# Kernel optimization log

Measured on AMD Instinct MI355X. Metric: run time of the kernel, lower is better.

Reference implementation:

```python
import jax, jax.numpy as jnp
import numpy as np

IN_NODES, OUT_NODES, F_SIZE = 4096, 1024, 16


def setup_inputs() -> dict:
    key = jax.random.key(0)
    u_hat = jax.random.normal(key, (IN_NODES * OUT_NODES, F_SIZE), dtype=jnp.float32)
    return {"u_hat": u_hat, "routing_num": 3}


def squash(s):
    # s: [out, f]
    sq = jnp.sum(s * s, axis=1, keepdims=True)
    return sq / (1.0 + sq) * (s / jnp.sqrt(sq))


def reference(u_hat, routing_num):
    # u_hat laid out edge-major as (in_node, out_node) blocks, matching DGL edge order
    uh = u_hat.reshape(IN_NODES, OUT_NODES, F_SIZE)
    b0 = jnp.zeros((IN_NODES, OUT_NODES), dtype=u_hat.dtype)

    def step(b, _):
        c = jax.nn.softmax(b, axis=1)                 # coupling coeffs over out capsules
        s = jnp.einsum('io,iof->of', c, uh)           # weighted message sum per out node
        v = squash(s)                                 # [out, f]
        b = b + jnp.einsum('iof,of->io', uh, v)       # agreement b-update
        return b, v

    _, vs = jax.lax.scan(step, b0, None, length=routing_num)
    return vs[-1]  # final out-capsule activations [OUT_NODES, F_SIZE]
```

## Files before the change

### kernel.cpp

```cpp
#include <hip/hip_runtime.h>
#include <math.h>

#define IN_NODES  4096
#define OUT_NODES 1024
#define FSZ       16
#define ROW_ELEMS (OUT_NODES * FSZ)

__device__ __forceinline__ float dot4(const float4 a, const float4 b) {
    return a.x*b.x + a.y*b.y + a.z*b.z + a.w*b.w;
}
__device__ __forceinline__ void fma4(float4& a, const float c, const float4 u) {
    a.x += c*u.x; a.y += c*u.y; a.z += c*u.z; a.w += c*u.w;
}
__device__ __forceinline__ void add4(float4& a, const float4 u) {
    a.x += u.x; a.y += u.y; a.z += u.z; a.w += u.w;
}

template <bool UNIFORM>
__global__ __launch_bounds__(1024) void route_pass(const float* __restrict__ uh,
                                                   const float* __restrict__ V,
                                                   float* __restrict__ s_partial,
                                                   int per_block) {
    const int t    = threadIdx.x;
    const int wave = t >> 6;
    const int lane = t & 63;
    const int c4   = (wave << 8) + lane;

    __shared__ float2 redw[16];
    __shared__ float2 redS;

    float4 v0, v1, v2, v3;
    if (!UNIFORM) {
        const float4* vp = reinterpret_cast<const float4*>(V) + c4;
        v0 = vp[0]; v1 = vp[64]; v2 = vp[128]; v3 = vp[192];
    }

    float4 a0 = make_float4(0.f,0.f,0.f,0.f), a1 = a0, a2 = a0, a3 = a0;

    const int i0 = blockIdx.x * per_block;
    for (int g = 0; g < per_block; g += 2) {
        const float4* pa = reinterpret_cast<const float4*>(
                               uh + (size_t)(i0 + g) * ROW_ELEMS) + c4;
        const float4* pb = pa + (ROW_ELEMS / 4);
        float4 ua0 = pa[0], ua1 = pa[64], ua2 = pa[128], ua3 = pa[192];
        float4 ub0 = pb[0], ub1 = pb[64], ub2 = pb[128], ub3 = pb[192];

        if (UNIFORM) {
            add4(a0, ua0); add4(a0, ub0);
            add4(a1, ua1); add4(a1, ub1);
            add4(a2, ua2); add4(a2, ub2);
            add4(a3, ua3); add4(a3, ub3);
        } else {
            float da0 = dot4(ua0, v0), da1 = dot4(ua1, v1),
                  da2 = dot4(ua2, v2), da3 = dot4(ua3, v3);
            float db0 = dot4(ub0, v0), db1 = dot4(ub1, v1),
                  db2 = dot4(ub2, v2), db3 = dot4(ub3, v3);
            da0 += __shfl_xor(da0, 1); da0 += __shfl_xor(da0, 2);
            da1 += __shfl_xor(da1, 1); da1 += __shfl_xor(da1, 2);
            da2 += __shfl_xor(da2, 1); da2 += __shfl_xor(da2, 2);
            da3 += __shfl_xor(da3, 1); da3 += __shfl_xor(da3, 2);
            db0 += __shfl_xor(db0, 1); db0 += __shfl_xor(db0, 2);
            db1 += __shfl_xor(db1, 1); db1 += __shfl_xor(db1, 2);
            db2 += __shfl_xor(db2, 1); db2 += __shfl_xor(db2, 2);
            db3 += __shfl_xor(db3, 1); db3 += __shfl_xor(db3, 2);

            float ea0 = __expf(da0), ea1 = __expf(da1),
                  ea2 = __expf(da2), ea3 = __expf(da3);
            float eb0 = __expf(db0), eb1 = __expf(db1),
                  eb2 = __expf(db2), eb3 = __expf(db3);

            float sx = (ea0 + ea1) + (ea2 + ea3);
            float sy = (eb0 + eb1) + (eb2 + eb3);
            #pragma unroll
            for (int off = 32; off; off >>= 1) {
                sx += __shfl_xor(sx, off);
                sy += __shfl_xor(sy, off);
            }
            if (lane == 0) redw[wave] = make_float2(sx, sy);
            __syncthreads();
            if (wave == 0) {
                float2 q = (lane < 16) ? redw[lane] : make_float2(0.f, 0.f);
                #pragma unroll
                for (int off = 8; off; off >>= 1) {
                    q.x += __shfl_xor(q.x, off);
                    q.y += __shfl_xor(q.y, off);
                }
                if (lane == 0) redS = q;
            }
            __syncthreads();
            const float inva = 4.0f / redS.x;
            const float invb = 4.0f / redS.y;

            fma4(a0, ea0 * inva, ua0); fma4(a0, eb0 * invb, ub0);
            fma4(a1, ea1 * inva, ua1); fma4(a1, eb1 * invb, ub1);
            fma4(a2, ea2 * inva, ua2); fma4(a2, eb2 * invb, ub2);
            fma4(a3, ea3 * inva, ua3); fma4(a3, eb3 * invb, ub3);
        }
    }

    if (UNIFORM) {
        const float c = 1.0f / OUT_NODES;
        a0.x*=c; a0.y*=c; a0.z*=c; a0.w*=c;
        a1.x*=c; a1.y*=c; a1.z*=c; a1.w*=c;
        a2.x*=c; a2.y*=c; a2.z*=c; a2.w*=c;
        a3.x*=c; a3.y*=c; a3.z*=c; a3.w*=c;
    }

    float4* sp = reinterpret_cast<float4*>(
                     s_partial + (size_t)blockIdx.x * ROW_ELEMS) + c4;
    sp[0] = a0; sp[64] = a1; sp[128] = a2; sp[192] = a3;
}

__global__ __launch_bounds__(256) void reduce_squash(const float* __restrict__ s_partial,
                                                     float* __restrict__ V,
                                                     float* __restrict__ out,
                                                     int nblk, int first) {
    const int gidx = blockIdx.x * 256 + threadIdx.x;
    float s0 = 0.f, s1 = 0.f, s2 = 0.f, s3 = 0.f;
    int b = 0;
    for (; b + 3 < nblk; b += 4) {
        s0 += s_partial[(size_t)(b    ) * ROW_ELEMS + gidx];
        s1 += s_partial[(size_t)(b + 1) * ROW_ELEMS + gidx];
        s2 += s_partial[(size_t)(b + 2) * ROW_ELEMS + gidx];
        s3 += s_partial[(size_t)(b + 3) * ROW_ELEMS + gidx];
    }
    for (; b < nblk; ++b)
        s0 += s_partial[(size_t)b * ROW_ELEMS + gidx];
    float s = (s0 + s1) + (s2 + s3);

    float sq = s * s;
    #pragma unroll
    for (int m = 8; m; m >>= 1)
        sq += __shfl_xor(sq, m);

    float scale = sq / ((1.0f + sq) * sqrtf(sq));
    float v = s * scale;

    out[gidx] = v;
    V[gidx]   = first ? v : (V[gidx] + v);
}

extern "C" void kernel_launch(void* const* d_in, const int* in_sizes, int n_in,
                              void* d_out, int out_size, void* d_ws, size_t ws_size,
                              hipStream_t stream) {
    const float* uh  = (const float*)d_in[0];
    float*       out = (float*)d_out;

    char*  ws   = (char*)d_ws;
    float* V    = (float*)ws;
    float* part = (float*)(ws + 65536);

    int G = 256;
    while (G > 1 && ws_size < 65536ull * (size_t)(G + 1)) G >>= 1;
    const int per_block = IN_NODES / G;

    route_pass<true><<<G, 1024, 0, stream>>>(uh, V, part, per_block);
    reduce_squash<<<64, 256, 0, stream>>>(part, V, out, G, 1);

    for (int t = 1; t < 3; ++t) {
        route_pass<false><<<G, 1024, 0, stream>>>(uh, V, part, per_block);
        reduce_squash<<<64, 256, 0, stream>>>(part, V, out, G, 0);
    }
}
```

Measured before the change: 195.9 us.

## Stream a bf16 copy of u_hat for the softmax routing passes

The first (uniform) pass now also writes a bf16 copy of u_hat into the workspace. The two later softmax-weighted passes read that half-size copy instead of the fp32 input, with register double-buffering of the next rows. The goal is to cut HBM traffic on the passes limited by memory bandwidth. The cost is an extra 128MB write in pass one and bf16 rounding error in the dot products and weighted sums. If the workspace is too small, the code falls back to the fp32 path.

Result: no change. 197.3 us (+0.7%).

```diff
diff --git a/kernel.cpp b/kernel.cpp
--- a/kernel.cpp
+++ b/kernel.cpp
@@ -3,8 +3,11 @@
 
 #define IN_NODES  4096
 #define OUT_NODES 1024
-#define FSZ       16
-#define ROW_ELEMS (OUT_NODES * FSZ)
+#define ROW_ELEMS (OUT_NODES * 16)
+#define ROW_C4    (ROW_ELEMS / 4)
+
+typedef unsigned short u16;
+typedef unsigned int   u32;
 
 __device__ __forceinline__ float dot4(const float4 a, const float4 b) {
     return a.x*b.x + a.y*b.y + a.z*b.z + a.w*b.w;
@@ -15,12 +18,60 @@
 __device__ __forceinline__ void add4(float4& a, const float4 u) {
     a.x += u.x; a.y += u.y; a.z += u.z; a.w += u.w;
 }
-
-template <bool UNIFORM>
-__global__ __launch_bounds__(1024) void route_pass(const float* __restrict__ uh,
-                                                   const float* __restrict__ V,
-                                                   float* __restrict__ s_partial,
-                                                   int per_block) {
+__device__ __forceinline__ float b2f1(u16 u) {
+    return __uint_as_float(((u32)u) << 16);
+}
+__device__ __forceinline__ float4 b2f(ushort4 u) {
+    return make_float4(b2f1(u.x), b2f1(u.y), b2f1(u.z), b2f1(u.w));
+}
+__device__ __forceinline__ u16 f2b(float x) {
+    u32 b = __float_as_uint(x);
+    return (u16)((b + 0x7FFFu + ((b >> 16) & 1u)) >> 16);
+}
+__device__ __forceinline__ ushort4 f2b4(float4 v) {
+    ushort4 r; r.x = f2b(v.x); r.y = f2b(v.y); r.z = f2b(v.z); r.w = f2b(v.w);
+    return r;
+}
+
+template <bool WBF16>
+__global__ __launch_bounds__(1024) void route_uniform(const float* __restrict__ uh,
+                                                      float* __restrict__ s_partial,
+                                                      u16* __restrict__ uh2,
+                                                      int per_block) {
+    const int t  = threadIdx.x;
+    const int c4 = ((t >> 6) << 8) + (t & 63);
+
+    float4 a0 = make_float4(0.f,0.f,0.f,0.f), a1 = a0, a2 = a0, a3 = a0;
+
+    const int i0 = blockIdx.x * per_block;
+    const float4* p = reinterpret_cast<const float4*>(uh) + (size_t)i0 * ROW_C4 + c4;
+    ushort4*      q = reinterpret_cast<ushort4*>(uh2)     + (size_t)i0 * ROW_C4 + c4;
+
+    for (int g = 0; g < per_block; ++g) {
+        float4 u0 = p[0], u1 = p[64], u2 = p[128], u3 = p[192];
+        add4(a0, u0); add4(a1, u1); add4(a2, u2); add4(a3, u3);
+        if (WBF16) {
+            q[0]   = f2b4(u0); q[64]  = f2b4(u1);
+            q[128] = f2b4(u2); q[192] = f2b4(u3);
+            q += ROW_C4;
+        }
+        p += ROW_C4;
+    }
+
+    const float c = 1.0f / OUT_NODES;
+    a0.x*=c; a0.y*=c; a0.z*=c; a0.w*=c;
+    a1.x*=c; a1.y*=c; a1.z*=c; a1.w*=c;
+    a2.x*=c; a2.y*=c; a2.z*=c; a2.w*=c;
+    a3.x*=c; a3.y*=c; a3.z*=c; a3.w*=c;
+
+    float4* sp = reinterpret_cast<float4*>(s_partial) + (size_t)blockIdx.x * ROW_C4 + c4;
+    sp[0] = a0; sp[64] = a1; sp[128] = a2; sp[192] = a3;
+}
+
+__global__ __launch_bounds__(1024) void route_soft_bf16(const u16* __restrict__ uh2,
+                                                        const float* __restrict__ V,
+                                                        float* __restrict__ s_partial,
+                                                        int per_block) {
     const int t    = threadIdx.x;
     const int wave = t >> 6;
     const int lane = t & 63;
@@ -29,85 +80,158 @@
     __shared__ float2 redw[16];
     __shared__ float2 redS;
 
-    float4 v0, v1, v2, v3;
-    if (!UNIFORM) {
-        const float4* vp = reinterpret_cast<const float4*>(V) + c4;
-        v0 = vp[0]; v1 = vp[64]; v2 = vp[128]; v3 = vp[192];
-    }
+    const float4* vp = reinterpret_cast<const float4*>(V) + c4;
+    const float4 v0 = vp[0], v1 = vp[64], v2 = vp[128], v3 = vp[192];
+
+    float4 a0 = make_float4(0.f,0.f,0.f,0.f), a1 = a0, a2 = a0, a3 = a0;
+
+    const ushort4* p = reinterpret_cast<const ushort4*>(uh2)
+                     + (size_t)(blockIdx.x * per_block) * ROW_C4 + c4;
+
+    ushort4 ca0 = p[0], ca1 = p[64], ca2 = p[128], ca3 = p[192];
+    const ushort4* pb = p + ROW_C4;
+    ushort4 cb0 = pb[0], cb1 = pb[64], cb2 = pb[128], cb3 = pb[192];
+
+    for (int g = 0; g < per_block; g += 2) {
+        ushort4 na0, na1, na2, na3, nb0, nb1, nb2, nb3;
+        const ushort4* pn = p + 2 * ROW_C4;
+        if (g + 2 < per_block) {
+            na0 = pn[0]; na1 = pn[64]; na2 = pn[128]; na3 = pn[192];
+            const ushort4* pn2 = pn + ROW_C4;
+            nb0 = pn2[0]; nb1 = pn2[64]; nb2 = pn2[128]; nb3 = pn2[192];
+        }
+
+        const float4 fa0 = b2f(ca0), fa1 = b2f(ca1), fa2 = b2f(ca2), fa3 = b2f(ca3);
+        const float4 fb0 = b2f(cb0), fb1 = b2f(cb1), fb2 = b2f(cb2), fb3 = b2f(cb3);
+
+        float da0 = dot4(fa0, v0), da1 = dot4(fa1, v1),
+              da2 = dot4(fa2, v2), da3 = dot4(fa3, v3);
+        float db0 = dot4(fb0, v0), db1 = dot4(fb1, v1),
+              db2 = dot4(fb2, v2), db3 = dot4(fb3, v3);
+
+        da0 += __shfl_xor(da0, 1); da0 += __shfl_xor(da0, 2);
+        da1 += __shfl_xor(da1, 1); da1 += __shfl_xor(da1, 2);
+        da2 += __shfl_xor(da2, 1); da2 += __shfl_xor(da2, 2);
+        da3 += __shfl_xor(da3, 1); da3 += __shfl_xor(da3, 2);
+        db0 += __shfl_xor(db0, 1); db0 += __shfl_xor(db0, 2);
+        db1 += __shfl_xor(db1, 1); db1 += __shfl_xor(db1, 2);
+        db2 += __shfl_xor(db2, 1); db2 += __shfl_xor(db2, 2);
+        db3 += __shfl_xor(db3, 1); db3 += __shfl_xor(db3, 2);
+
+        float ea0 = __expf(da0), ea1 = __expf(da1),
+              ea2 = __expf(da2), ea3 = __expf(da3);
+        float eb0 = __expf(db0), eb1 = __expf(db1),
+              eb2 = __expf(db2), eb3 = __expf(db3);
+
+        float sx = (ea0 + ea1) + (ea2 + ea3);
+        float sy = (eb0 + eb1) + (eb2 + eb3);
+        #pragma unroll
+        for (int off = 32; off; off >>= 1) {
+            sx += __shfl_xor(sx, off);
+            sy += __shfl_xor(sy, off);
+        }
+        if (lane == 0) redw[wave] = make_float2(sx, sy);
+        __syncthreads();
+        if (wave == 0) {
+            float2 qv = (lane < 16) ? redw[lane] : make_float2(0.f, 0.f);
+            #pragma unroll
+            for (int off = 8; off; off >>= 1) {
+                qv.x += __shfl_xor(qv.x, off);
+                qv.y += __shfl_xor(qv.y, off);
+            }
+            if (lane == 0) redS = qv;
+        }
+        __syncthreads();
+        const float inva = 4.0f / redS.x;
+        const float invb = 4.0f / redS.y;
+
+        fma4(a0, ea0 * inva, fa0); fma4(a0, eb0 * invb, fb0);
+        fma4(a1, ea1 * inva, fa1); fma4(a1, eb1 * invb, fb1);
+        fma4(a2, ea2 * inva, fa2); fma4(a2, eb2 * invb, fb2);
+        fma4(a3, ea3 * inva, fa3); fma4(a3, eb3 * invb, fb3);
+
+        ca0 = na0; ca1 = na1; ca2 = na2; ca3 = na3;
+        cb0 = nb0; cb1 = nb1; cb2 = nb2; cb3 = nb3;
+        p = pn;
+    }
+
+    float4* sp = reinterpret_cast<float4*>(s_partial) + (size_t)blockIdx.x * ROW_C4 + c4;
+    sp[0] = a0; sp[64] = a1; sp[128] = a2; sp[192] = a3;
+}
+
+__global__ __launch_bounds__(1024) void route_soft_f32(const float* __restrict__ uh,
+                                                       const float* __restrict__ V,
+                                                       float* __restrict__ s_partial,
+                                                       int per_block) {
+    const int t    = threadIdx.x;
+    const int wave = t >> 6;
+    const int lane = t & 63;
+    const int c4   = (wave << 8) + lane;
+
+    __shared__ float2 redw[16];
+    __shared__ float2 redS;
+
+    const float4* vp = reinterpret_cast<const float4*>(V) + c4;
+    const float4 v0 = vp[0], v1 = vp[64], v2 = vp[128], v3 = vp[192];
 
     float4 a0 = make_float4(0.f,0.f,0.f,0.f), a1 = a0, a2 = a0, a3 = a0;
 
     const int i0 = blockIdx.x * per_block;
     for (int g = 0; g < per_block; g += 2) {
-        const float4* pa = reinterpret_cast<const float4*>(
-                               uh + (size_t)(i0 + g) * ROW_ELEMS) + c4;
-        const float4* pb = pa + (ROW_ELEMS / 4);
+        const float4* pa = reinterpret_cast<const float4*>(uh)
+                         + (size_t)(i0 + g) * ROW_C4 + c4;
+        const float4* pb = pa + ROW_C4;
         float4 ua0 = pa[0], ua1 = pa[64], ua2 = pa[128], ua3 = pa[192];
         float4 ub0 = pb[0], ub1 = pb[64], ub2 = pb[128], ub3 = pb[192];
 
-        if (UNIFORM) {
-            add4(a0, ua0); add4(a0, ub0);
-            add4(a1, ua1); add4(a1, ub1);
-            add4(a2, ua2); add4(a2, ub2);
-            add4(a3, ua3); add4(a3, ub3);
-        } else {
-            float da0 = dot4(ua0, v0), da1 = dot4(ua1, v1),
-                  da2 = dot4(ua2, v2), da3 = dot4(ua3, v3);
-            float db0 = dot4(ub0, v0), db1 = dot4(ub1, v1),
-                  db2 = dot4(ub2, v2), db3 = dot4(ub3, v3);
-            da0 += __shfl_xor(da0, 1); da0 += __shfl_xor(da0, 2);
-            da1 += __shfl_xor(da1, 1); da1 += __shfl_xor(da1, 2);
-            da2 += __shfl_xor(da2, 1); da2 += __shfl_xor(da2, 2);
-            da3 += __shfl_xor(da3, 1); da3 += __shfl_xor(da3, 2);
-            db0 += __shfl_xor(db0, 1); db0 += __shfl_xor(db0, 2);
-            db1 += __shfl_xor(db1, 1); db1 += __shfl_xor(db1, 2);
-            db2 += __shfl_xor(db2, 1); db2 += __shfl_xor(db2, 2);
-            db3 += __shfl_xor(db3, 1); db3 += __shfl_xor(db3, 2);
-
-            float ea0 = __expf(da0), ea1 = __expf(da1),
-                  ea2 = __expf(da2), ea3 = __expf(da3);
-            float eb0 = __expf(db0), eb1 = __expf(db1),
-                  eb2 = __expf(db2), eb3 = __expf(db3);
-
-            float sx = (ea0 + ea1) + (ea2 + ea3);
-            float sy = (eb0 + eb1) + (eb2 + eb3);
+        float da0 = dot4(ua0, v0), da1 = dot4(ua1, v1),
+              da2 = dot4(ua2, v2), da3 = dot4(ua3, v3);
+        float db0 = dot4(ub0, v0), db1 = dot4(ub1, v1),
+              db2 = dot4(ub2, v2), db3 = dot4(ub3, v3);
+
+        da0 += __shfl_xor(da0, 1); da0 += __shfl_xor(da0, 2);
+        da1 += __shfl_xor(da1, 1); da1 += __shfl_xor(da1, 2);
+        da2 += __shfl_xor(da2, 1); da2 += __shfl_xor(da2, 2);
+        da3 += __shfl_xor(da3, 1); da3 += __shfl_xor(da3, 2);
+        db0 += __shfl_xor(db0, 1); db0 += __shfl_xor(db0, 2);
+        db1 += __shfl_xor(db1, 1); db1 += __shfl_xor(db1, 2);
+        db2 += __shfl_xor(db2, 1); db2 += __shfl_xor(db2, 2);
+        db3 += __shfl_xor(db3, 1); db3 += __shfl_xor(db3, 2);
+
+        float ea0 = __expf(da0), ea1 = __expf(da1),
+              ea2 = __expf(da2), ea3 = __expf(da3);
+        float eb0 = __expf(db0), eb1 = __expf(db1),
+              eb2 = __expf(db2), eb3 = __expf(db3);
+
+        float sx = (ea0 + ea1) + (ea2 + ea3);
+        float sy = (eb0 + eb1) + (eb2 + eb3);
+        #pragma unroll
+        for (int off = 32; off; off >>= 1) {
+            sx += __shfl_xor(sx, off);
+            sy += __shfl_xor(sy, off);
+        }
+        if (lane == 0) redw[wave] = make_float2(sx, sy);
+        __syncthreads();
+        if (wave == 0) {
+            float2 qv = (lane < 16) ? redw[lane] : make_float2(0.f, 0.f);
             #pragma unroll
-            for (int off = 32; off; off >>= 1) {
-                sx += __shfl_xor(sx, off);
-                sy += __shfl_xor(sy, off);
+            for (int off = 8; off; off >>= 1) {
+                qv.x += __shfl_xor(qv.x, off);
+                qv.y += __shfl_xor(qv.y, off);
             }
-            if (lane == 0) redw[wave] = make_float2(sx, sy);
-            __syncthreads();
-            if (wave == 0) {
-                float2 q = (lane < 16) ? redw[lane] : make_float2(0.f, 0.f);
-                #pragma unroll
-                for (int off = 8; off; off >>= 1) {
-                    q.x += __shfl_xor(q.x, off);
-                    q.y += __shfl_xor(q.y, off);
-                }
-                if (lane == 0) redS = q;
-            }
-            __syncthreads();
-            const float inva = 4.0f / redS.x;
-            const float invb = 4.0f / redS.y;
-
-            fma4(a0, ea0 * inva, ua0); fma4(a0, eb0 * invb, ub0);
-            fma4(a1, ea1 * inva, ua1); fma4(a1, eb1 * invb, ub1);
-            fma4(a2, ea2 * inva, ua2); fma4(a2, eb2 * invb, ub2);
-            fma4(a3, ea3 * inva, ua3); fma4(a3, eb3 * invb, ub3);
-        }
-    }
-
-    if (UNIFORM) {
-        const float c = 1.0f / OUT_NODES;
-        a0.x*=c; a0.y*=c; a0.z*=c; a0.w*=c;
-        a1.x*=c; a1.y*=c; a1.z*=c; a1.w*=c;
-        a2.x*=c; a2.y*=c; a2.z*=c; a2.w*=c;
-        a3.x*=c; a3.y*=c; a3.z*=c; a3.w*=c;
-    }
-
-    float4* sp = reinterpret_cast<float4*>(
-                     s_partial + (size_t)blockIdx.x * ROW_ELEMS) + c4;
+            if (lane == 0) redS = qv;
+        }
+        __syncthreads();
+        const float inva = 4.0f / redS.x;
+        const float invb = 4.0f / redS.y;
+
+        fma4(a0, ea0 * inva, ua0); fma4(a0, eb0 * invb, ub0);
+        fma4(a1, ea1 * inva, ua1); fma4(a1, eb1 * invb, ub1);
+        fma4(a2, ea2 * inva, ua2); fma4(a2, eb2 * invb, ub2);
+        fma4(a3, ea3 * inva, ua3); fma4(a3, eb3 * invb, ub3);
+    }
+
+    float4* sp = reinterpret_cast<float4*>(s_partial) + (size_t)blockIdx.x * ROW_C4 + c4;
     sp[0] = a0; sp[64] = a1; sp[128] = a2; sp[192] = a3;
 }
 
@@ -151,14 +275,30 @@
     float* part = (float*)(ws + 65536);
 
     int G = 256;
-    while (G > 1 && ws_size < 65536ull * (size_t)(G + 1)) G >>= 1;
-    const int per_block = IN_NODES / G;
-
-    route_pass<true><<<G, 1024, 0, stream>>>(uh, V, part, per_block);
-    reduce_squash<<<64, 256, 0, stream>>>(part, V, out, G, 1);
-
-    for (int t = 1; t < 3; ++t) {
-        route_pass<false><<<G, 1024, 0, stream>>>(uh, V, part, per_block);
-        reduce_squash<<<64, 256, 0, stream>>>(part, V, out, G, 0);
-    }
-}
+    const size_t need_bf16 = 65536ull * 257ull + (size_t)IN_NODES * ROW_ELEMS * 2ull;
+    const bool use_bf16 = (ws_size >= need_bf16);
+
+    if (use_bf16) {
+        u16* uh2 = (u16*)(ws + 65536ull * 257ull);
+        const int per_block = IN_NODES / G;
+
+        route_uniform<true><<<G, 1024, 0, stream>>>(uh, part, uh2, per_block);
+        reduce_squash<<<64, 256, 0, stream>>>(part, V, out, G, 1);
+
+        for (int it = 1; it < 3; ++it) {
+            route_soft_bf16<<<G, 1024, 0, stream>>>(uh2, V, part, per_block);
+            reduce_squash<<<64, 256, 0, stream>>>(part, V, out, G, 0);
+        }
+    } else {
+        while (G > 1 && ws_size < 65536ull * (size_t)(G + 1)) G >>= 1;
+        const int per_block = IN_NODES / G;
+
+        route_uniform<false><<<G, 1024, 0, stream>>>(uh, part, nullptr, per_block);
+        reduce_squash<<<64, 256, 0, stream>>>(part, V, out, G, 1);
+
+        for (int it = 1; it < 3; ++it) {
+            route_soft_f32<<<G, 1024, 0, stream>>>(uh, V, part, per_block);
+            reduce_squash<<<64, 256, 0, stream>>>(part, V, out, G, 0);
+        }
+    }
+}
```
